# Optimization experiments

Measured on AMD Instinct MI355X. Metric: run time of the kernel, lower is better.

## Reference

```python
import jax, jax.numpy as jnp
import numpy as np

TAU = 1.0
EPS = 1e-8


def setup_inputs() -> dict:
    key = jax.random.key(0)
    ks = jax.random.split(key, 9)
    B, S, D, R, T = 32, 512, 768, 16, 10
    return {
        "x": jax.random.normal(ks[0], (B, S, D), jnp.float32),
        "A_q": jax.random.normal(ks[1], (T, R, D), jnp.float32),
        "B_q": jax.random.normal(ks[2], (T, D, R), jnp.float32),
        "A_v": jax.random.normal(ks[3], (T, R, D), jnp.float32),
        "B_v": jax.random.normal(ks[4], (T, D, R), jnp.float32),
        "qkv_w": jax.random.normal(ks[5], (3 * D, D), jnp.float32) * 0.02,
        "qkv_b": jax.random.normal(ks[6], (3 * D,), jnp.float32) * 0.02,
        "gate_logits": jax.random.normal(ks[7], (T,), jnp.float32),
        "alpha": jax.random.normal(ks[8], (T,), jnp.float32),
    }


def _delta(x, A, B, coef):
    # A: [T,r,d] (torch Linear weight), B: [T,d,r]
    # per-adapter normalized output: (x @ A_t^T @ B_t^T) / (||A_t||_F * ||B_t||_F + eps)
    norm = (jnp.sqrt(jnp.sum(A * A, axis=(1, 2)))
            * jnp.sqrt(jnp.sum(B * B, axis=(1, 2))) + EPS)  # [T]
    w = coef / norm  # [T], folds beta_t * alpha_t / norm_t into the contraction
    h = jnp.einsum('bsd,trd->bstr', x, A)          # [B,S,T,r] tiny rank intermediate
    return jnp.einsum('bstr,t,tdr->bsd', h, w, B)  # weighted sum over tasks


def reference(x, A_q, B_q, A_v, B_v, qkv_w, qkv_b, gate_logits, alpha):
    # deterministic gate: beta = softmax(logits / tau) (Gumbel noise omitted for a
    # reproducible reference of delta = sum_t beta_t * alpha_t * normalized_adapter_t)
    beta = jax.nn.softmax(gate_logits / TAU)
    coef = beta * alpha
    delta_q = _delta(x, A_q, B_q, coef)
    delta_v = _delta(x, A_v, B_v, coef)
    qkv = jnp.einsum('bsd,ed->bse', x, qkv_w) + qkv_b  # [B,S,3D]
    D = x.shape[-1]
    qkv = qkv.at[..., :D].add(delta_q)
    qkv = qkv.at[..., -D:].add(delta_v)
    return qkv
```

## Files before the change

kernel.cpp:

```cpp
#include <hip/hip_runtime.h>

typedef unsigned short u16;
typedef unsigned int   u32;
typedef __bf16 bf16x8 __attribute__((ext_vector_type(8)));
typedef float  f32x4  __attribute__((ext_vector_type(4)));

#define M_TOT 16384
#define K_TOT 768
#define N_TOT 2304

__device__ __forceinline__ u16 f32_to_bf16(float f) {
  u32 u = __float_as_uint(f);
  u32 r = (u + 0x7FFFu + ((u >> 16) & 1u)) >> 16;
  return (u16)r;
}
__device__ __forceinline__ float bf16_to_f32(u16 h) {
  return __uint_as_float(((u32)h) << 16);
}

__device__ __forceinline__ void gload_lds16(const void* gsrc, void* lds) {
  __builtin_amdgcn_global_load_lds(
      (const __attribute__((address_space(1))) void*)gsrc,
      (__attribute__((address_space(3))) void*)lds, 16, 0, 0);
}

__global__ void norms_kernel(const float* __restrict__ Aq, const float* __restrict__ Bq,
                             const float* __restrict__ Av, const float* __restrict__ Bv,
                             float* __restrict__ sumsq) {
  int b = blockIdx.x;
  int which = b / 10, t = b % 10;
  const float* src =
      (which == 0 ? Aq : which == 1 ? Bq : which == 2 ? Av : Bv) + t * 12288;
  float s = 0.f;
  for (int i = threadIdx.x; i < 12288; i += 256) { float v = src[i]; s += v * v; }
  for (int off = 32; off > 0; off >>= 1) s += __shfl_down(s, off, 64);
  __shared__ float red[4];
  if ((threadIdx.x & 63) == 0) red[threadIdx.x >> 6] = s;
  __syncthreads();
  if (threadIdx.x == 0) sumsq[b] = red[0] + red[1] + red[2] + red[3];
}

__global__ void weights_kernel(const float* __restrict__ logits, const float* __restrict__ alpha,
                               const float* __restrict__ sumsq,
                               float* __restrict__ wq, float* __restrict__ wv) {
  int t = threadIdx.x;
  if (t >= 10) return;
  float m = -1e30f;
  for (int i = 0; i < 10; ++i) m = fmaxf(m, logits[i]);
  float sum = 0.f;
  for (int i = 0; i < 10; ++i) sum += expf(logits[i] - m);
  float coef = (expf(logits[t] - m) / sum) * alpha[t];
  wq[t] = coef / (sqrtf(sumsq[t])      * sqrtf(sumsq[10 + t]) + 1e-8f);
  wv[t] = coef / (sqrtf(sumsq[20 + t]) * sqrtf(sumsq[30 + t]) + 1e-8f);
}

__global__ __launch_bounds__(256) void build_weff(
    const float* __restrict__ qkv_w,
    const float* __restrict__ Aq, const float* __restrict__ Bq,
    const float* __restrict__ Av, const float* __restrict__ Bv,
    const float* __restrict__ wq, const float* __restrict__ wv,
    u16* __restrict__ Whi, u16* __restrict__ Wlo) {
  __shared__ float As[160][64];
  __shared__ float Bs[160][32];
  __shared__ float wsh[16];

  const int k0 = blockIdx.x * 64;
  const int n0 = blockIdx.y * 32;
  const int tid = threadIdx.x;
  const int nl = tid >> 3;
  const int kg = tid & 7;

  float acc[8] = {0, 0, 0, 0, 0, 0, 0, 0};
  const bool is_q = (n0 < 768);
  const bool is_v = (n0 >= 1536);
  if (is_q || is_v) {
    const float* A  = is_q ? Aq : Av;
    const float* Bm = is_q ? Bq : Bv;
    const float* w  = is_q ? wq : wv;
    const int noff = is_q ? n0 : (n0 - 1536);
    for (int i = tid; i < 10240; i += 256)
      As[i >> 6][i & 63] = A[(i >> 6) * 768 + k0 + (i & 63)];
    for (int i = tid; i < 5120; i += 256) {
      int tr = i >> 5, n = i & 31;
      Bs[tr][n] = Bm[(tr >> 4) * 12288 + (noff + n) * 16 + (tr & 15)];
    }
    if (tid < 10) wsh[tid] = w[tid];
    __syncthreads();
    for (int tr = 0; tr < 160; ++tr) {
      float wb = wsh[tr >> 4] * Bs[tr][nl];
#pragma unroll
      for (int j = 0; j < 8; ++j) acc[j] += wb * As[tr][kg * 8 + j];
    }
  }
  const int n = n0 + nl;
  const size_t base = (size_t)n * 768 + k0 + kg * 8;
#pragma unroll
  for (int j = 0; j < 8; ++j) {
    float v = qkv_w[base + j] + acc[j];
    u16 h = f32_to_bf16(v);
    u16 l = f32_to_bf16(v - bf16_to_f32(h));
    Whi[base + j] = h;
    Wlo[base + j] = l;
  }
}

__global__ void split_x(const float* __restrict__ x, u16* __restrict__ Xhi, u16* __restrict__ Xlo) {
  int i4 = blockIdx.x * 256 + threadIdx.x;
  if (i4 >= 3145728) return;
  float4 v = ((const float4*)x)[i4];
  u32 h0 = f32_to_bf16(v.x), h1 = f32_to_bf16(v.y), h2 = f32_to_bf16(v.z), h3 = f32_to_bf16(v.w);
  u32 l0 = f32_to_bf16(v.x - bf16_to_f32((u16)h0));
  u32 l1 = f32_to_bf16(v.y - bf16_to_f32((u16)h1));
  u32 l2 = f32_to_bf16(v.z - bf16_to_f32((u16)h2));
  u32 l3 = f32_to_bf16(v.w - bf16_to_f32((u16)h3));
  ((uint2*)Xhi)[i4] = make_uint2(h0 | (h1 << 16), h2 | (h3 << 16));
  ((uint2*)Xlo)[i4] = make_uint2(l0 | (l1 << 16), l2 | (l3 << 16));
}

__global__ __launch_bounds__(256) void gemm_split3(
    const u16* __restrict__ Xhi, const u16* __restrict__ Xlo,
    const u16* __restrict__ Whi, const u16* __restrict__ Wlo,
    const float* __restrict__ bias, float* __restrict__ out) {
  __shared__ __align__(16) u16 lds[4 * 128 * 32];
  u16* xs_hi = lds;
  u16* xs_lo = lds + 4096;
  u16* ws_hi = lds + 8192;
  u16* ws_lo = lds + 12288;

  const int tid  = threadIdx.x;
  const int lane = tid & 63;
  const int wid  = tid >> 6;
  const int m0 = blockIdx.y << 7;
  const int n0 = blockIdx.x << 7;
  const int wm = ((wid >> 1) & 1) << 6;
  const int wn = (wid & 1) << 6;

  const int idxA = tid, idxB = tid + 256;
  const int rA = idxA >> 2, sA = idxA & 3;
  const int rB = idxB >> 2, sB = idxB & 3;
  const size_t offXA = (size_t)(m0 + rA) * 768 + ((sA ^ (rA & 3)) << 3);
  const size_t offXB = (size_t)(m0 + rB) * 768 + ((sB ^ (rB & 3)) << 3);
  const size_t offWA = (size_t)(n0 + rA) * 768 + ((sA ^ (rA & 3)) << 3);
  const size_t offWB = (size_t)(n0 + rB) * 768 + ((sB ^ (rB & 3)) << 3);
  const int ldsA = wid * 512;
  const int ldsB = wid * 512 + 2048;

  const int fl = lane & 15, fs = lane >> 4;
  int aoff[4], boff[4];
#pragma unroll
  for (int i = 0; i < 4; ++i) {
    int rm = wm + i * 16 + fl;
    aoff[i] = rm * 32 + ((fs ^ (rm & 3)) << 3);
    int rn = wn + i * 16 + fl;
    boff[i] = rn * 32 + ((fs ^ (rn & 3)) << 3);
  }

  f32x4 acc[4][4] = {};

  for (int step = 0; step < 24; ++step) {
    const int k0 = step << 5;
    gload_lds16(Xhi + offXA + k0, xs_hi + ldsA);
    gload_lds16(Xhi + offXB + k0, xs_hi + ldsB);
    gload_lds16(Xlo + offXA + k0, xs_lo + ldsA);
    gload_lds16(Xlo + offXB + k0, xs_lo + ldsB);
    gload_lds16(Whi + offWA + k0, ws_hi + ldsA);
    gload_lds16(Whi + offWB + k0, ws_hi + ldsB);
    gload_lds16(Wlo + offWA + k0, ws_lo + ldsA);
    gload_lds16(Wlo + offWB + k0, ws_lo + ldsB);
    __syncthreads();

    bf16x8 ah[4], al[4], bh[4], bl[4];
#pragma unroll
    for (int i = 0; i < 4; ++i) {
      ah[i] = *(const bf16x8*)(xs_hi + aoff[i]);
      al[i] = *(const bf16x8*)(xs_lo + aoff[i]);
      bh[i] = *(const bf16x8*)(ws_hi + boff[i]);
      bl[i] = *(const bf16x8*)(ws_lo + boff[i]);
    }
#pragma unroll
    for (int i = 0; i < 4; ++i)
#pragma unroll
      for (int j = 0; j < 4; ++j) {
        acc[i][j] = __builtin_amdgcn_mfma_f32_16x16x32_bf16(ah[i], bh[j], acc[i][j], 0, 0, 0);
        acc[i][j] = __builtin_amdgcn_mfma_f32_16x16x32_bf16(ah[i], bl[j], acc[i][j], 0, 0, 0);
        acc[i][j] = __builtin_amdgcn_mfma_f32_16x16x32_bf16(al[i], bh[j], acc[i][j], 0, 0, 0);
      }
    __syncthreads();
  }

#pragma unroll
  for (int j = 0; j < 4; ++j) {
    const int n = n0 + wn + j * 16 + fl;
    const float bj = bias[n];
#pragma unroll
    for (int i = 0; i < 4; ++i) {
      const int mbase = m0 + wm + i * 16 + (fs << 2);
#pragma unroll
      for (int r = 0; r < 4; ++r)
        out[(size_t)(mbase + r) * N_TOT + n] = acc[i][j][r] + bj;
    }
  }
}

extern "C" void kernel_launch(void* const* d_in, const int* in_sizes, int n_in,
                              void* d_out, int out_size, void* d_ws, size_t ws_size,
                              hipStream_t stream) {
  const float* x     = (const float*)d_in[0];
  const float* Aq    = (const float*)d_in[1];
  const float* Bq    = (const float*)d_in[2];
  const float* Av    = (const float*)d_in[3];
  const float* Bv    = (const float*)d_in[4];
  const float* qkvw  = (const float*)d_in[5];
  const float* qkvb  = (const float*)d_in[6];
  const float* gate  = (const float*)d_in[7];
  const float* alpha = (const float*)d_in[8];
  float* out = (float*)d_out;

  char* ws = (char*)d_ws;
  float* sumsq = (float*)ws;
  float* wq    = (float*)(ws + 256);
  float* wv    = (float*)(ws + 512);
  u16* Whi = (u16*)(ws + 1024);
  u16* Wlo = Whi + 1769472;
  u16* Xhi = Wlo + 1769472;
  u16* Xlo = Xhi + 12582912;

  hipLaunchKernelGGL(norms_kernel,   dim3(40),      dim3(256), 0, stream, Aq, Bq, Av, Bv, sumsq);
  hipLaunchKernelGGL(weights_kernel, dim3(1),       dim3(64),  0, stream, gate, alpha, sumsq, wq, wv);
  hipLaunchKernelGGL(build_weff,     dim3(12, 72),  dim3(256), 0, stream, qkvw, Aq, Bq, Av, Bv, wq, wv, Whi, Wlo);
  hipLaunchKernelGGL(split_x,        dim3(12288),   dim3(256), 0, stream, x, Xhi, Xlo);
  hipLaunchKernelGGL(gemm_split3,    dim3(18, 128), dim3(256), 0, stream, Xhi, Xlo, Whi, Wlo, qkvb, out);
}
```

Measured before the change: 430.7 us.

## Rewrite split-bf16 GEMM with 256x256 tiles and a four-buffer async pipeline

Replaces the 128x128 split-precision GEMM with a 512-thread kernel using 256x256 output tiles. The hi/lo products become three sequential K-passes (72 steps) over a four-slot, 128KB dynamic-LDS ring, prefetching two steps ahead with vmcnt waits and a single barrier per step. It also adds grouped block swizzling for L2 reuse and raised wave priority around the MFMA burst. The aim is more data reuse per tile and overlap of global-to-LDS loads with matrix math, at the cost of large LDS use (one block per CU) and fewer blocks (576).

```diff
diff --git a/kernel.cpp b/kernel.cpp
--- a/kernel.cpp
+++ b/kernel.cpp
@@ -5,8 +5,6 @@
 typedef __bf16 bf16x8 __attribute__((ext_vector_type(8)));
 typedef float  f32x4  __attribute__((ext_vector_type(4)));
 
-#define M_TOT 16384
-#define K_TOT 768
 #define N_TOT 2304
 
 __device__ __forceinline__ u16 f32_to_bf16(float f) {
@@ -117,75 +115,97 @@
   ((uint2*)Xlo)[i4] = make_uint2(l0 | (l1 << 16), l2 | (l3 << 16));
 }
 
-__global__ __launch_bounds__(256) void gemm_split3(
+__global__ __launch_bounds__(512, 2) void gemm_kc(
     const u16* __restrict__ Xhi, const u16* __restrict__ Xlo,
     const u16* __restrict__ Whi, const u16* __restrict__ Wlo,
     const float* __restrict__ bias, float* __restrict__ out) {
-  __shared__ __align__(16) u16 lds[4 * 128 * 32];
-  u16* xs_hi = lds;
-  u16* xs_lo = lds + 4096;
-  u16* ws_hi = lds + 8192;
-  u16* ws_lo = lds + 12288;
+  extern __shared__ char smem[];
 
   const int tid  = threadIdx.x;
   const int lane = tid & 63;
   const int wid  = tid >> 6;
-  const int m0 = blockIdx.y << 7;
-  const int n0 = blockIdx.x << 7;
-  const int wm = ((wid >> 1) & 1) << 6;
-  const int wn = (wid & 1) << 6;
-
-  const int idxA = tid, idxB = tid + 256;
-  const int rA = idxA >> 2, sA = idxA & 3;
-  const int rB = idxB >> 2, sB = idxB & 3;
-  const size_t offXA = (size_t)(m0 + rA) * 768 + ((sA ^ (rA & 3)) << 3);
-  const size_t offXB = (size_t)(m0 + rB) * 768 + ((sB ^ (rB & 3)) << 3);
-  const size_t offWA = (size_t)(n0 + rA) * 768 + ((sA ^ (rA & 3)) << 3);
-  const size_t offWB = (size_t)(n0 + rB) * 768 + ((sB ^ (rB & 3)) << 3);
-  const int ldsA = wid * 512;
-  const int ldsB = wid * 512 + 2048;
-
+
+  const int bid = blockIdx.x;
+  const int swz = (bid & 7) * 72 + (bid >> 3);
+  const int m0 = (swz / 9) << 8;
+  const int n0 = (swz % 9) << 8;
+
+  const int wm = (wid >> 2) << 7;
+  const int wn = (wid & 3) << 6;
   const int fl = lane & 15, fs = lane >> 4;
-  int aoff[4], boff[4];
-#pragma unroll
-  for (int i = 0; i < 4; ++i) {
-    int rm = wm + i * 16 + fl;
-    aoff[i] = rm * 32 + ((fs ^ (rm & 3)) << 3);
-    int rn = wn + i * 16 + fl;
-    boff[i] = rn * 32 + ((fs ^ (rn & 3)) << 3);
-  }
-
-  f32x4 acc[4][4] = {};
-
-  for (int step = 0; step < 24; ++step) {
-    const int k0 = step << 5;
-    gload_lds16(Xhi + offXA + k0, xs_hi + ldsA);
-    gload_lds16(Xhi + offXB + k0, xs_hi + ldsB);
-    gload_lds16(Xlo + offXA + k0, xs_lo + ldsA);
-    gload_lds16(Xlo + offXB + k0, xs_lo + ldsB);
-    gload_lds16(Whi + offWA + k0, ws_hi + ldsA);
-    gload_lds16(Whi + offWB + k0, ws_hi + ldsB);
-    gload_lds16(Wlo + offWA + k0, ws_lo + ldsA);
-    gload_lds16(Wlo + offWB + k0, ws_lo + ldsB);
-    __syncthreads();
-
-    bf16x8 ah[4], al[4], bh[4], bl[4];
-#pragma unroll
-    for (int i = 0; i < 4; ++i) {
-      ah[i] = *(const bf16x8*)(xs_hi + aoff[i]);
-      al[i] = *(const bf16x8*)(xs_lo + aoff[i]);
-      bh[i] = *(const bf16x8*)(ws_hi + boff[i]);
-      bl[i] = *(const bf16x8*)(ws_lo + boff[i]);
-    }
-#pragma unroll
-    for (int i = 0; i < 4; ++i)
-#pragma unroll
-      for (int j = 0; j < 4; ++j) {
-        acc[i][j] = __builtin_amdgcn_mfma_f32_16x16x32_bf16(ah[i], bh[j], acc[i][j], 0, 0, 0);
-        acc[i][j] = __builtin_amdgcn_mfma_f32_16x16x32_bf16(ah[i], bl[j], acc[i][j], 0, 0, 0);
-        acc[i][j] = __builtin_amdgcn_mfma_f32_16x16x32_bf16(al[i], bh[j], acc[i][j], 0, 0, 0);
-      }
-    __syncthreads();
+
+  int aFrag[8], bFrag[4];
+#pragma unroll
+  for (int i = 0; i < 8; ++i) {
+    int R = wm + i * 16 + fl;
+    int pr = R >> 1;
+    int u = (fs + ((R & 1) << 2)) ^ (pr & 7);
+    aFrag[i] = (pr * 8 + u) * 16;
+  }
+#pragma unroll
+  for (int j = 0; j < 4; ++j) {
+    int R = wn + j * 16 + fl;
+    int pr = R >> 1;
+    int u = (fs + ((R & 1) << 2)) ^ (pr & 7);
+    bFrag[j] = (pr * 8 + u) * 16;
+  }
+
+  int ldsByte[2];
+  long aSrcOff[2], bSrcOff[2];
+#pragma unroll
+  for (int jj = 0; jj < 2; ++jj) {
+    int P = jj * 512 + tid;
+    int pr = P >> 3, p = P & 7;
+    int u = p ^ (pr & 7);
+    int r = (pr << 1) | (u >> 2);
+    int s = u & 3;
+    ldsByte[jj]  = P * 16;
+    aSrcOff[jj] = (long)(m0 + r) * 768 + s * 8;
+    bSrcOff[jj] = (long)(n0 + r) * 768 + s * 8;
+  }
+
+  auto stage = [&](int t2, int bufi) {
+    int tc = t2 > 71 ? 71 : t2;
+    int reg = tc / 24;
+    int ksrc = (tc - reg * 24) << 5;
+    const u16* xb = (reg == 2) ? Xlo : Xhi;
+    const u16* wb = (reg == 1) ? Wlo : Whi;
+    char* base = smem + bufi * 32768;
+    gload_lds16(xb + aSrcOff[0] + ksrc, base + ldsByte[0]);
+    gload_lds16(xb + aSrcOff[1] + ksrc, base + ldsByte[1]);
+    gload_lds16(wb + bSrcOff[0] + ksrc, base + 16384 + ldsByte[0]);
+    gload_lds16(wb + bSrcOff[1] + ksrc, base + 16384 + ldsByte[1]);
+  };
+
+  f32x4 acc[8][4] = {};
+
+  stage(0, 0);
+  stage(1, 1);
+  asm volatile("s_waitcnt vmcnt(4)" ::: "memory");
+  __builtin_amdgcn_sched_barrier(0);
+  __builtin_amdgcn_s_barrier();
+
+  for (int t = 0; t < 72; ++t) {
+    char* bufA = smem + (t & 3) * 32768;
+    char* bufB = bufA + 16384;
+    bf16x8 a[8], b[4];
+#pragma unroll
+    for (int i = 0; i < 8; ++i) a[i] = *(const bf16x8*)(bufA + aFrag[i]);
+#pragma unroll
+    for (int j = 0; j < 4; ++j) b[j] = *(const bf16x8*)(bufB + bFrag[j]);
+
+    stage(t + 2, (t + 2) & 3);
+    asm volatile("s_waitcnt vmcnt(4)" ::: "memory");
+    __builtin_amdgcn_sched_barrier(0);
+    __builtin_amdgcn_s_barrier();
+
+    __builtin_amdgcn_s_setprio(1);
+#pragma unroll
+    for (int i = 0; i < 8; ++i)
+#pragma unroll
+      for (int j = 0; j < 4; ++j)
+        acc[i][j] = __builtin_amdgcn_mfma_f32_16x16x32_bf16(a[i], b[j], acc[i][j], 0, 0, 0);
+    __builtin_amdgcn_s_setprio(0);
   }
 
 #pragma unroll
@@ -193,7 +213,7 @@
     const int n = n0 + wn + j * 16 + fl;
     const float bj = bias[n];
 #pragma unroll
-    for (int i = 0; i < 4; ++i) {
+    for (int i = 0; i < 8; ++i) {
       const int mbase = m0 + wm + i * 16 + (fs << 2);
 #pragma unroll
       for (int r = 0; r < 4; ++r)
@@ -225,9 +245,17 @@
   u16* Xhi = Wlo + 1769472;
   u16* Xlo = Xhi + 12582912;
 
-  hipLaunchKernelGGL(norms_kernel,   dim3(40),      dim3(256), 0, stream, Aq, Bq, Av, Bv, sumsq);
-  hipLaunchKernelGGL(weights_kernel, dim3(1),       dim3(64),  0, stream, gate, alpha, sumsq, wq, wv);
-  hipLaunchKernelGGL(build_weff,     dim3(12, 72),  dim3(256), 0, stream, qkvw, Aq, Bq, Av, Bv, wq, wv, Whi, Wlo);
-  hipLaunchKernelGGL(split_x,        dim3(12288),   dim3(256), 0, stream, x, Xhi, Xlo);
-  hipLaunchKernelGGL(gemm_split3,    dim3(18, 128), dim3(256), 0, stream, Xhi, Xlo, Whi, Wlo, qkvb, out);
-}
+  static bool attr_set = false;
+  if (!attr_set) {
+    hipFuncSetAttribute((const void*)gemm_kc,
+                        hipFuncAttributeMaxDynamicSharedMemorySize, 131072);
+    attr_set = true;
+  }
+
+  hipLaunchKernelGGL(norms_kernel,   dim3(40),     dim3(256), 0, stream, Aq, Bq, Av, Bv, sumsq);
+  hipLaunchKernelGGL(weights_kernel, dim3(1),      dim3(64),  0, stream, gate, alpha, sumsq, wq, wv);
+  hipLaunchKernelGGL(build_weff,     dim3(12, 72), dim3(256), 0, stream, qkvw, Aq, Bq, Av, Bv, wq, wv, Whi, Wlo);
+  hipLaunchKernelGGL(split_x,        dim3(12288),  dim3(256), 0, stream, x, Xhi, Xlo);
+  hipLaunchKernelGGL(gemm_kc,        dim3(576),    dim3(512), 131072, stream,
+                     Xhi, Xlo, Whi, Wlo, qkvb, out);
+}
```

After: 447.4 us. +3.9%, slower.
